# Kernel optimization log

Hardware: AMD Instinct MI355X
Metric: run time of the kernel (lower is better)

## Reference

```python
import jax, jax.numpy as jnp
import numpy as np

N, D_IN, D_H, N_HEADS, N_CLS = 8192, 384, 64, 4, 6
LN_EPS = 1e-5


def setup_inputs() -> dict:
    key = jax.random.key(0)
    ks = jax.random.split(key, 8)
    x = jax.random.normal(ks[0], (N, D_IN), dtype=jnp.float32)
    proj_w = jax.random.normal(ks[1], (D_IN, D_H), dtype=jnp.float32) / np.sqrt(D_IN)
    proj_b = jnp.zeros((D_H,), jnp.float32)
    head_w = jax.random.normal(ks[2], (N_HEADS, D_H, D_H), dtype=jnp.float32) / np.sqrt(D_H)
    head_b = jnp.zeros((N_HEADS, D_H), jnp.float32)
    attn_w = jnp.ones((N_HEADS,), jnp.float32)  # nn.Parameter(torch.ones(num_heads))
    gamma = jnp.ones((D_H,), jnp.float32)
    beta = jnp.zeros((D_H,), jnp.float32)
    fc_w = jax.random.normal(ks[3], (D_H, N_CLS), dtype=jnp.float32) / np.sqrt(D_H)
    fc_b = jnp.zeros((N_CLS,), jnp.float32)
    return {"x": x, "proj_w": proj_w, "proj_b": proj_b, "head_w": head_w,
            "head_b": head_b, "attn_w": attn_w, "gamma": gamma, "beta": beta,
            "fc_w": fc_w, "fc_b": fc_b}


def _safe_cdist_sq_to_dist(sq):
    # Euclidean distance with zero (sub)gradient at zero distance, matching torch.cdist.
    pos = sq > 0
    return jnp.where(pos, jnp.sqrt(jnp.where(pos, sq, 1.0)), 0.0)


def reference(x, proj_w, proj_b, head_w, head_b, attn_w, gamma, beta, fc_w, fc_b):
    h = jax.nn.relu(x @ proj_w + proj_b)                      # [N, D_H]
    hp = jnp.einsum('nd,hde->hne', h, head_w) + head_b[:, None, :]  # [H, N, D_H]
    sumsq = jnp.sum(hp * hp, axis=-1)                          # [H, N]
    sq = sumsq[:, :, None] + sumsq[:, None, :] - 2.0 * jnp.einsum('hnd,hmd->hnm', hp, hp)
    dist = _safe_cdist_sq_to_dist(jnp.maximum(sq, 0.0))        # [H, N, N]
    scores = jax.nn.softmax(-dist, axis=-1)                    # [H, N, N]
    h_head = jnp.einsum('hnm,hmd->hnd', scores, hp)            # [H, N, D_H]
    aw = jax.nn.softmax(attn_w, axis=0)                        # [H]
    combined = jnp.einsum('h,hnd->nd', aw, h_head)             # [N, D_H]
    mu = jnp.mean(combined, axis=-1, keepdims=True)
    var = jnp.mean((combined - mu) ** 2, axis=-1, keepdims=True)
    normed = (combined - mu) * jax.lax.rsqrt(var + LN_EPS) * gamma + beta
    return normed @ fc_w + fc_b                                # [N, N_CLS]
```

## Files before the change

### kernel.cpp

```cpp
#include <hip/hip_runtime.h>

#define N_TOK 8192
#define D_IN 384
#define D_H 64
#define NHEADS 4
#define NSPLIT 3
#define N_CLS 6
#define LN_EPS 1e-5f

typedef __attribute__((ext_vector_type(8))) short short8;
typedef __attribute__((ext_vector_type(4))) float f32x4;

#define L2E2 2.08136898100560774f

__device__ __forceinline__ unsigned short f2bf(float f) {
    unsigned int u = __float_as_uint(f);
    u += 0x7FFFu + ((u >> 16) & 1u);
    return (unsigned short)(u >> 16);
}
__device__ __forceinline__ float bf2f(unsigned short s) {
    return __uint_as_float(((unsigned int)s) << 16);
}

__device__ __forceinline__ int kperm(int k) {
    return (k & 32) + 2 * (k & 15) + ((k >> 4) & 1);
}

__global__ __launch_bounds__(512) void stage1_kernel(
    const float* __restrict__ x, const float* __restrict__ proj_w,
    const float* __restrict__ proj_b, const float* __restrict__ head_w,
    const float* __restrict__ head_b,
    unsigned short* __restrict__ hp, unsigned short* __restrict__ Vf,
    float* __restrict__ ssq2)
{
    const int lane = threadIdx.x & 63;
    const int wv   = threadIdx.x >> 6;
    const int rb0  = blockIdx.x * 32;

    __shared__ float h_sh[32][68];
    __shared__ __align__(16) unsigned short vt[NHEADS][4][64][8];

    {
        float acc[4];
        float b = proj_b[lane];
        #pragma unroll
        for (int r = 0; r < 4; ++r) acc[r] = b;
        const float* x0 = x + (size_t)(rb0 + wv * 4) * D_IN;
        #pragma unroll 2
        for (int k4 = 0; k4 < D_IN / 4; ++k4) {
            float w0 = proj_w[(k4 * 4 + 0) * 64 + lane];
            float w1 = proj_w[(k4 * 4 + 1) * 64 + lane];
            float w2 = proj_w[(k4 * 4 + 2) * 64 + lane];
            float w3 = proj_w[(k4 * 4 + 3) * 64 + lane];
            #pragma unroll
            for (int r = 0; r < 4; ++r) {
                float4 xv = *(const float4*)(x0 + r * D_IN + k4 * 4);
                acc[r] = fmaf(xv.x, w0, acc[r]);
                acc[r] = fmaf(xv.y, w1, acc[r]);
                acc[r] = fmaf(xv.z, w2, acc[r]);
                acc[r] = fmaf(xv.w, w3, acc[r]);
            }
        }
        #pragma unroll
        for (int r = 0; r < 4; ++r)
            h_sh[wv * 4 + r][lane] = fmaxf(acc[r], 0.f);
    }
    __syncthreads();

    const int head = wv >> 1;
    const int half = wv & 1;
    float a[16];
    {
        float b = head_b[head * 64 + lane];
        #pragma unroll
        for (int r = 0; r < 16; ++r) a[r] = b;
    }
    const float* wb = head_w + head * 64 * 64;
    #pragma unroll 2
    for (int e4 = 0; e4 < 16; ++e4) {
        float w0 = wb[(e4 * 4 + 0) * 64 + lane];
        float w1 = wb[(e4 * 4 + 1) * 64 + lane];
        float w2 = wb[(e4 * 4 + 2) * 64 + lane];
        float w3 = wb[(e4 * 4 + 3) * 64 + lane];
        #pragma unroll
        for (int r = 0; r < 16; ++r) {
            float4 hv = *(const float4*)&h_sh[half * 16 + r][e4 * 4];
            a[r] = fmaf(hv.x, w0, a[r]);
            a[r] = fmaf(hv.y, w1, a[r]);
            a[r] = fmaf(hv.z, w2, a[r]);
            a[r] = fmaf(hv.w, w3, a[r]);
        }
    }

    #pragma unroll
    for (int r = 0; r < 16; ++r) {
        int kl  = half * 16 + r;
        int row = rb0 + kl;
        unsigned short hb = f2bf(a[r]);
        float hf = bf2f(hb);
        hp[((size_t)head * N_TOK + row) * 64 + lane] = hb;
        int p = kperm(row & 63);
        vt[head][(p >> 3) & 3][lane][p & 7] = hb;
        float s = hf * hf;
        #pragma unroll
        for (int off = 32; off > 0; off >>= 1) s += __shfl_xor(s, off);
        if (lane == 0) ssq2[head * N_TOK + row] = s * L2E2;
    }
    __syncthreads();

    const int kgbase = (rb0 & 32) ? 4 : 0;
    #pragma unroll
    for (int i = 0; i < 2; ++i) {
        int c  = threadIdx.x + 512 * i;
        int hc = c >> 8, rem = c & 255;
        int kg = rem >> 6, d = rem & 63;
        short8 v = *(const short8*)&vt[hc][kg][d][0];
        *(short8*)&Vf[(((size_t)hc * (N_TOK / 8) + (rb0 >> 6) * 8 + kgbase + kg) * 64
                       + d) * 8] = v;
    }
}

__global__ __launch_bounds__(256, 4) void flash_kernel(
    const unsigned short* __restrict__ hp, const unsigned short* __restrict__ Vf,
    const float* __restrict__ ssq2, unsigned short* __restrict__ Og,
    float* __restrict__ Lg)
{
    const int head  = blockIdx.x & 3;
    const int split = blockIdx.x >> 2;
    const int q0    = blockIdx.y * 128;
    const int w     = threadIdx.x >> 6;
    const int lane  = threadIdx.x & 63;
    const int col   = lane & 15;
    const int quad  = lane >> 4;
    const int tid   = threadIdx.x;

    __shared__ __align__(16) unsigned short Psh[4][2][16][72];
    __shared__ __align__(16) unsigned short Kst[2][4096];
    __shared__ __align__(16) unsigned short Vst[2][4096];

    const unsigned short* hpH = hp + head * (N_TOK * 64);
    const unsigned short* VfH = Vf + head * (N_TOK * 64);
    const float* ssqH = ssq2 + head * N_TOK;

    const int rb = q0 + w * 32;
    const bool diag_lo = ((rb >> 5) & 1) == 0;

    short8 aQ[2][2];
    float ssqn2[2][4];
    #pragma unroll
    for (int s = 0; s < 2; ++s) {
        const unsigned short* qrow = hpH + (rb + s * 16 + col) * 64;
        aQ[s][0] = *(const short8*)(qrow + quad * 8);
        aQ[s][1] = *(const short8*)(qrow + 32 + quad * 8);
        #pragma unroll
        for (int r = 0; r < 4; ++r)
            ssqn2[s][r] = ssqH[rb + s * 16 + quad * 4 + r];
    }

    const f32x4 zero4 = {0.f, 0.f, 0.f, 0.f};
    f32x4 accO[2][4] = {{zero4, zero4, zero4, zero4}, {zero4, zero4, zero4, zero4}};
    f32x4 accL[2] = {zero4, zero4};
    const short8 ones = {16256,16256,16256,16256,16256,16256,16256,16256};
    const float NEG2L2 = -2.0f * L2E2;

    const int koff0 = (((tid & ~7) | ((tid & 7) ^ ((tid >> 3) & 7))) << 4);
    const int karow = col * 128 + ((quad ^ (col & 7)) << 4);
    const int va    = (quad * 64 + col) << 4;

    const int kt0   = (split * 128) / NSPLIT;
    const int ktend = ((split + 1) * 128) / NSPLIT;

    short8 stK0, stK1, stV0, stV1;
    {
        const unsigned short* kg = hpH + kt0 * 4096;
        const unsigned short* vg = VfH + kt0 * 4096;
        stK0 = *(const short8*)(kg + tid * 8);
        stK1 = *(const short8*)(kg + tid * 8 + 2048);
        stV0 = *(const short8*)(vg + tid * 8);
        stV1 = *(const short8*)(vg + tid * 8 + 2048);
        *(short8*)((char*)&Kst[0][0] + koff0)        = stK0;
        *(short8*)((char*)&Kst[0][0] + koff0 + 4096) = stK1;
        *(short8*)((char*)&Vst[0][0] + tid * 16)        = stV0;
        *(short8*)((char*)&Vst[0][0] + tid * 16 + 4096) = stV1;
    }
    float smc[4];
    #pragma unroll
    for (int nt = 0; nt < 4; ++nt) smc[nt] = ssqH[kt0 * 64 + nt * 16 + col];
    __syncthreads();

    #pragma unroll 1
    for (int kt = kt0; kt < ktend; ++kt) {
        const int b = (kt - kt0) & 1;
        const char* Kb = (const char*)&Kst[b][0];
        const char* Vb = (const char*)&Vst[b][0];
        const bool has_next = (kt + 1 < ktend);

        float smn[4];
        if (has_next) {
            const unsigned short* kg = hpH + (kt + 1) * 4096;
            const unsigned short* vg = VfH + (kt + 1) * 4096;
            stK0 = *(const short8*)(kg + tid * 8);
            stK1 = *(const short8*)(kg + tid * 8 + 2048);
            stV0 = *(const short8*)(vg + tid * 8);
            stV1 = *(const short8*)(vg + tid * 8 + 2048);
            #pragma unroll
            for (int nt = 0; nt < 4; ++nt)
                smn[nt] = ssqH[(kt + 1) * 64 + nt * 16 + col];
        }

        f32x4 aSA[2][2] = {{zero4, zero4}, {zero4, zero4}};
        {
            short8 k0 = *(const short8*)(Kb + karow);
            short8 k1 = *(const short8*)(Kb + (karow ^ 64));
            short8 k2 = *(const short8*)(Kb + 2048 + karow);
            short8 k3 = *(const short8*)(Kb + 2048 + (karow ^ 64));
            aSA[0][0] = __builtin_amdgcn_mfma_f32_16x16x32_bf16(aQ[0][0], k0, aSA[0][0], 0, 0, 0);
            aSA[0][0] = __builtin_amdgcn_mfma_f32_16x16x32_bf16(aQ[0][1], k1, aSA[0][0], 0, 0, 0);
            aSA[1][0] = __builtin_amdgcn_mfma_f32_16x16x32_bf16(aQ[1][0], k0, aSA[1][0], 0, 0, 0);
            aSA[1][0] = __builtin_amdgcn_mfma_f32_16x16x32_bf16(aQ[1][1], k1, aSA[1][0], 0, 0, 0);
            aSA[0][1] = __builtin_amdgcn_mfma_f32_16x16x32_bf16(aQ[0][0], k2, aSA[0][1], 0, 0, 0);
            aSA[0][1] = __builtin_amdgcn_mfma_f32_16x16x32_bf16(aQ[0][1], k3, aSA[0][1], 0, 0, 0);
            aSA[1][1] = __builtin_amdgcn_mfma_f32_16x16x32_bf16(aQ[1][0], k2, aSA[1][1], 0, 0, 0);
            aSA[1][1] = __builtin_amdgcn_mfma_f32_16x16x32_bf16(aQ[1][1], k3, aSA[1][1], 0, 0, 0);
        }

        #pragma unroll
        for (int s = 0; s < 2; ++s) {
            float pf0[4], pf1[4];
            #pragma unroll
            for (int r = 0; r < 4; ++r) {
                float sq0 = fmaf(aSA[s][0][r], NEG2L2, ssqn2[s][r] + smc[0]);
                pf0[r] = __builtin_amdgcn_exp2f(-__builtin_amdgcn_sqrtf(fmaxf(sq0, 0.f)));
                float sq1 = fmaf(aSA[s][1][r], NEG2L2, ssqn2[s][r] + smc[1]);
                pf1[r] = __builtin_amdgcn_exp2f(-__builtin_amdgcn_sqrtf(fmaxf(sq1, 0.f)));
            }
            #pragma unroll
            for (int r = 0; r < 4; ++r) {
                unsigned int d0 = __builtin_amdgcn_perm(__float_as_uint(pf1[r]),
                                                        __float_as_uint(pf0[r]), 0x07060302u);
                *(unsigned int*)&Psh[w][s][quad * 4 + r][2 * col] = d0;
            }
        }
        if (diag_lo && kt == (rb >> 6) && lane < 16) {
            #pragma unroll
            for (int s = 0; s < 2; ++s) {
                int t = ((rb + s * 16) >> 4) & 3;
                Psh[w][s][lane][2 * lane + (t & 1)] = 0x3F80;
            }
        }

        f32x4 aSB[2][2] = {{zero4, zero4}, {zero4, zero4}};
        {
            short8 k0 = *(const short8*)(Kb + 4096 + karow);
            short8 k1 = *(const short8*)(Kb + 4096 + (karow ^ 64));
            short8 k2 = *(const short8*)(Kb + 6144 + karow);
            short8 k3 = *(const short8*)(Kb + 6144 + (karow ^ 64));
            aSB[0][0] = __builtin_amdgcn_mfma_f32_16x16x32_bf16(aQ[0][0], k0, aSB[0][0], 0, 0, 0);
            aSB[0][0] = __builtin_amdgcn_mfma_f32_16x16x32_bf16(aQ[0][1], k1, aSB[0][0], 0, 0, 0);
            aSB[1][0] = __builtin_amdgcn_mfma_f32_16x16x32_bf16(aQ[1][0], k0, aSB[1][0], 0, 0, 0);
            aSB[1][0] = __builtin_amdgcn_mfma_f32_16x16x32_bf16(aQ[1][1], k1, aSB[1][0], 0, 0, 0);
            aSB[0][1] = __builtin_amdgcn_mfma_f32_16x16x32_bf16(aQ[0][0], k2, aSB[0][1], 0, 0, 0);
            aSB[0][1] = __builtin_amdgcn_mfma_f32_16x16x32_bf16(aQ[0][1], k3, aSB[0][1], 0, 0, 0);
            aSB[1][1] = __builtin_amdgcn_mfma_f32_16x16x32_bf16(aQ[1][0], k2, aSB[1][1], 0, 0, 0);
            aSB[1][1] = __builtin_amdgcn_mfma_f32_16x16x32_bf16(aQ[1][1], k3, aSB[1][1], 0, 0, 0);
        }

        #pragma unroll
        for (int s = 0; s < 2; ++s) {
            float pf2[4], pf3[4];
            #pragma unroll
            for (int r = 0; r < 4; ++r) {
                float sq2 = fmaf(aSB[s][0][r], NEG2L2, ssqn2[s][r] + smc[2]);
                pf2[r] = __builtin_amdgcn_exp2f(-__builtin_amdgcn_sqrtf(fmaxf(sq2, 0.f)));
                float sq3 = fmaf(aSB[s][1][r], NEG2L2, ssqn2[s][r] + smc[3]);
                pf3[r] = __builtin_amdgcn_exp2f(-__builtin_amdgcn_sqrtf(fmaxf(sq3, 0.f)));
            }
            #pragma unroll
            for (int r = 0; r < 4; ++r) {
                unsigned int d1 = __builtin_amdgcn_perm(__float_as_uint(pf3[r]),
                                                        __float_as_uint(pf2[r]), 0x07060302u);
                *(unsigned int*)&Psh[w][s][quad * 4 + r][32 + 2 * col] = d1;
            }
        }
        if (!diag_lo && kt == (rb >> 6) && lane < 16) {
            #pragma unroll
            for (int s = 0; s < 2; ++s) {
                int t = ((rb + s * 16) >> 4) & 3;
                Psh[w][s][lane][32 + 2 * lane + (t & 1)] = 0x3F80;
            }
        }

        {
            short8 aP0 = *(const short8*)&Psh[w][0][col][quad * 8];
            short8 aP1 = *(const short8*)&Psh[w][1][col][quad * 8];
            short8 bV[4];
            #pragma unroll
            for (int dt = 0; dt < 4; ++dt)
                bV[dt] = *(const short8*)(Vb + va + dt * 256);
            accL[0] = __builtin_amdgcn_mfma_f32_16x16x32_bf16(aP0, ones, accL[0], 0, 0, 0);
            accL[1] = __builtin_amdgcn_mfma_f32_16x16x32_bf16(aP1, ones, accL[1], 0, 0, 0);
            #pragma unroll
            for (int dt = 0; dt < 4; ++dt) {
                accO[0][dt] = __builtin_amdgcn_mfma_f32_16x16x32_bf16(aP0, bV[dt], accO[0][dt], 0, 0, 0);
                accO[1][dt] = __builtin_amdgcn_mfma_f32_16x16x32_bf16(aP1, bV[dt], accO[1][dt], 0, 0, 0);
            }
        }
        {
            short8 aP0b = *(const short8*)&Psh[w][0][col][32 + quad * 8];
            short8 aP1b = *(const short8*)&Psh[w][1][col][32 + quad * 8];
            short8 bV[4];
            #pragma unroll
            for (int dt = 0; dt < 4; ++dt)
                bV[dt] = *(const short8*)(Vb + va + dt * 256 + 4096);
            accL[0] = __builtin_amdgcn_mfma_f32_16x16x32_bf16(aP0b, ones, accL[0], 0, 0, 0);
            accL[1] = __builtin_amdgcn_mfma_f32_16x16x32_bf16(aP1b, ones, accL[1], 0, 0, 0);
            #pragma unroll
            for (int dt = 0; dt < 4; ++dt) {
                accO[0][dt] = __builtin_amdgcn_mfma_f32_16x16x32_bf16(aP0b, bV[dt], accO[0][dt], 0, 0, 0);
                accO[1][dt] = __builtin_amdgcn_mfma_f32_16x16x32_bf16(aP1b, bV[dt], accO[1][dt], 0, 0, 0);
            }
        }

        if (has_next) {
            char* Kn = (char*)&Kst[b ^ 1][0];
            char* Vn = (char*)&Vst[b ^ 1][0];
            *(short8*)(Kn + koff0)        = stK0;
            *(short8*)(Kn + koff0 + 4096) = stK1;
            *(short8*)(Vn + tid * 16)        = stV0;
            *(short8*)(Vn + tid * 16 + 4096) = stV1;
        }
        __syncthreads();
        if (has_next) {
            smc[0] = smn[0]; smc[1] = smn[1]; smc[2] = smn[2]; smc[3] = smn[3];
        }
    }

    unsigned short* og = Og + (size_t)(split * NHEADS + head) * N_TOK * 64;
    float* lg = Lg + (size_t)(split * NHEADS + head) * N_TOK;
    #pragma unroll
    for (int s = 0; s < 2; ++s)
        #pragma unroll
        for (int r = 0; r < 4; ++r) {
            int row = rb + s * 16 + quad * 4 + r;
            #pragma unroll
            for (int dt = 0; dt < 4; ++dt)
                og[row * 64 + dt * 16 + col] = f2bf(accO[s][dt][r]);
            if (col == 0) lg[row] = accL[s][r];
        }
}

__global__ __launch_bounds__(256) void combine_kernel(
    const unsigned short* __restrict__ Og, const float* __restrict__ Lg,
    const float* __restrict__ attn_w, const float* __restrict__ gamma,
    const float* __restrict__ beta, const float* __restrict__ fc_w,
    const float* __restrict__ fc_b, float* __restrict__ out)
{
    const int lane = threadIdx.x & 63;
    const int ty   = threadIdx.x >> 6;
    const int row  = blockIdx.x * 4 + ty;

    float a0 = attn_w[0], a1 = attn_w[1], a2 = attn_w[2], a3 = attn_w[3];
    float m = fmaxf(fmaxf(a0, a1), fmaxf(a2, a3));
    float e0 = __expf(a0 - m), e1 = __expf(a1 - m), e2 = __expf(a2 - m), e3 = __expf(a3 - m);
    float inv = 1.f / (e0 + e1 + e2 + e3);
    float aw[4] = {e0 * inv, e1 * inv, e2 * inv, e3 * inv};

    float c = 0.f;
    #pragma unroll
    for (int hh = 0; hh < NHEADS; ++hh) {
        float l = 0.f, o = 0.f;
        #pragma unroll
        for (int s = 0; s < NSPLIT; ++s) {
            l += Lg[(s * NHEADS + hh) * N_TOK + row];
            o += bf2f(Og[(size_t)((s * NHEADS + hh) * N_TOK + row) * 64 + lane]);
        }
        c += aw[hh] * o * __builtin_amdgcn_rcpf(l);
    }

    float s = c;
    #pragma unroll
    for (int off = 32; off > 0; off >>= 1) s += __shfl_xor(s, off);
    float mu = s * (1.f / 64.f);
    float d = c - mu;
    float v = d * d;
    #pragma unroll
    for (int off = 32; off > 0; off >>= 1) v += __shfl_xor(v, off);
    float normed = d * rsqrtf(v * (1.f / 64.f) + LN_EPS) * gamma[lane] + beta[lane];

    float lg[N_CLS];
    #pragma unroll
    for (int cc = 0; cc < N_CLS; ++cc) {
        float p = normed * fc_w[lane * N_CLS + cc];
        #pragma unroll
        for (int off = 32; off > 0; off >>= 1) p += __shfl_xor(p, off);
        lg[cc] = p;
    }
    if (lane == 0) {
        #pragma unroll
        for (int cc = 0; cc < N_CLS; ++cc)
            out[row * N_CLS + cc] = lg[cc] + fc_b[cc];
    }
}

extern "C" void kernel_launch(void* const* d_in, const int* in_sizes, int n_in,
                              void* d_out, int out_size, void* d_ws, size_t ws_size,
                              hipStream_t stream)
{
    const float* x      = (const float*)d_in[0];
    const float* proj_w = (const float*)d_in[1];
    const float* proj_b = (const float*)d_in[2];
    const float* head_w = (const float*)d_in[3];
    const float* head_b = (const float*)d_in[4];
    const float* attn_w = (const float*)d_in[5];
    const float* gamma  = (const float*)d_in[6];
    const float* beta   = (const float*)d_in[7];
    const float* fc_w   = (const float*)d_in[8];
    const float* fc_b   = (const float*)d_in[9];
    float* out = (float*)d_out;

    char* ws = (char*)d_ws;
    unsigned short* hp = (unsigned short*)(ws);
    unsigned short* Vf = (unsigned short*)(ws + (4u << 20));
    float* ssq2 = (float*)(ws + (8u << 20));
    unsigned short* Og = (unsigned short*)(ws + (8u << 20) + (128u << 10));
    float* Lg   = (float*)(ws + (20u << 20) + (128u << 10));

    stage1_kernel<<<N_TOK / 32, 512, 0, stream>>>(x, proj_w, proj_b, head_w, head_b,
                                                  hp, Vf, ssq2);
    dim3 g2(NHEADS * NSPLIT, N_TOK / 128);
    flash_kernel<<<g2, 256, 0, stream>>>(hp, Vf, ssq2, Og, Lg);
    combine_kernel<<<N_TOK / 4, 256, 0, stream>>>(Og, Lg, attn_w, gamma, beta,
                                                  fc_w, fc_b, out);
}
```

Before: 229.4 us.

## Stream K/V tiles via direct global-to-LDS loads with single buffers and swizzled P

```diff
diff --git a/kernel.cpp b/kernel.cpp
--- a/kernel.cpp
+++ b/kernel.cpp
@@ -4,7 +4,7 @@
 #define D_IN 384
 #define D_H 64
 #define NHEADS 4
-#define NSPLIT 3
+#define NSPLIT 4
 #define N_CLS 6
 #define LN_EPS 1e-5f
 
@@ -24,6 +24,12 @@
 
 __device__ __forceinline__ int kperm(int k) {
     return (k & 32) + 2 * (k & 15) + ((k >> 4) & 1);
+}
+
+__device__ __forceinline__ void gload_lds16(const void* g, void* l) {
+    __builtin_amdgcn_global_load_lds(
+        (const __attribute__((address_space(1))) unsigned int*)g,
+        (__attribute__((address_space(3))) unsigned int*)l, 16, 0, 0);
 }
 
 __global__ __launch_bounds__(512) void stage1_kernel(
@@ -134,9 +140,9 @@
     const int quad  = lane >> 4;
     const int tid   = threadIdx.x;
 
-    __shared__ __align__(16) unsigned short Psh[4][2][16][72];
-    __shared__ __align__(16) unsigned short Kst[2][4096];
-    __shared__ __align__(16) unsigned short Vst[2][4096];
+    __shared__ __align__(16) unsigned short Psh[4][2][16][64];
+    __shared__ __align__(16) unsigned short Kst[4096];
+    __shared__ __align__(16) unsigned short Vst[4096];
 
     const unsigned short* hpH = hp + head * (N_TOK * 64);
     const unsigned short* VfH = Vf + head * (N_TOK * 64);
@@ -166,22 +172,16 @@
     const int koff0 = (((tid & ~7) | ((tid & 7) ^ ((tid >> 3) & 7))) << 4);
     const int karow = col * 128 + ((quad ^ (col & 7)) << 4);
     const int va    = (quad * 64 + col) << 4;
-
-    const int kt0   = (split * 128) / NSPLIT;
-    const int ktend = ((split + 1) * 128) / NSPLIT;
-
-    short8 stK0, stK1, stV0, stV1;
+    const int wcb   = quad * 512 + ((((col >> 2) ^ ((quad & 1) << 2)) << 4))
+                      + ((col & 3) << 2);
+
+    const int kt0   = split * 32;
+    const int ktend = kt0 + 32;
+
     {
-        const unsigned short* kg = hpH + kt0 * 4096;
-        const unsigned short* vg = VfH + kt0 * 4096;
-        stK0 = *(const short8*)(kg + tid * 8);
-        stK1 = *(const short8*)(kg + tid * 8 + 2048);
-        stV0 = *(const short8*)(vg + tid * 8);
-        stV1 = *(const short8*)(vg + tid * 8 + 2048);
-        *(short8*)((char*)&Kst[0][0] + koff0)        = stK0;
-        *(short8*)((char*)&Kst[0][0] + koff0 + 4096) = stK1;
-        *(short8*)((char*)&Vst[0][0] + tid * 16)        = stV0;
-        *(short8*)((char*)&Vst[0][0] + tid * 16 + 4096) = stV1;
+        const char* kg = (const char*)(hpH + kt0 * 4096);
+        gload_lds16(kg + koff0,        (char*)Kst + tid * 16);
+        gload_lds16(kg + koff0 + 4096, (char*)Kst + tid * 16 + 4096);
     }
     float smc[4];
     #pragma unroll
@@ -190,23 +190,21 @@
 
     #pragma unroll 1
     for (int kt = kt0; kt < ktend; ++kt) {
-        const int b = (kt - kt0) & 1;
-        const char* Kb = (const char*)&Kst[b][0];
-        const char* Vb = (const char*)&Vst[b][0];
         const bool has_next = (kt + 1 < ktend);
 
+        {
+            const char* vg = (const char*)(VfH + kt * 4096);
+            gload_lds16(vg + tid * 16,        (char*)Vst + tid * 16);
+            gload_lds16(vg + tid * 16 + 4096, (char*)Vst + tid * 16 + 4096);
+        }
         float smn[4];
         if (has_next) {
-            const unsigned short* kg = hpH + (kt + 1) * 4096;
-            const unsigned short* vg = VfH + (kt + 1) * 4096;
-            stK0 = *(const short8*)(kg + tid * 8);
-            stK1 = *(const short8*)(kg + tid * 8 + 2048);
-            stV0 = *(const short8*)(vg + tid * 8);
-            stV1 = *(const short8*)(vg + tid * 8 + 2048);
             #pragma unroll
             for (int nt = 0; nt < 4; ++nt)
                 smn[nt] = ssqH[(kt + 1) * 64 + nt * 16 + col];
         }
+
+        const char* Kb = (const char*)Kst;
 
         f32x4 aSA[2][2] = {{zero4, zero4}, {zero4, zero4}};
         {
@@ -226,6 +224,7 @@
 
         #pragma unroll
         for (int s = 0; s < 2; ++s) {
+            char* pB = (char*)&Psh[w][s][0][0];
             float pf0[4], pf1[4];
             #pragma unroll
             for (int r = 0; r < 4; ++r) {
@@ -238,14 +237,16 @@
             for (int r = 0; r < 4; ++r) {
                 unsigned int d0 = __builtin_amdgcn_perm(__float_as_uint(pf1[r]),
                                                         __float_as_uint(pf0[r]), 0x07060302u);
-                *(unsigned int*)&Psh[w][s][quad * 4 + r][2 * col] = d0;
+                *(unsigned int*)(pB + ((wcb ^ (r << 4)) + r * 128)) = d0;
             }
         }
         if (diag_lo && kt == (rb >> 6) && lane < 16) {
             #pragma unroll
             for (int s = 0; s < 2; ++s) {
                 int t = ((rb + s * 16) >> 4) & 3;
-                Psh[w][s][lane][2 * lane + (t & 1)] = 0x3F80;
+                int sc2 = 4 * lane + 2 * (t & 1);
+                int ad = lane * 128 + (((lane >> 2) ^ (lane & 7)) << 4) + (sc2 & 15);
+                *(unsigned short*)((char*)&Psh[w][s][0][0] + ad) = 0x3F80;
             }
         }
 
@@ -267,6 +268,7 @@
 
         #pragma unroll
         for (int s = 0; s < 2; ++s) {
+            char* pB = (char*)&Psh[w][s][0][0];
             float pf2[4], pf3[4];
             #pragma unroll
             for (int r = 0; r < 4; ++r) {
@@ -279,20 +281,33 @@
             for (int r = 0; r < 4; ++r) {
                 unsigned int d1 = __builtin_amdgcn_perm(__float_as_uint(pf3[r]),
                                                         __float_as_uint(pf2[r]), 0x07060302u);
-                *(unsigned int*)&Psh[w][s][quad * 4 + r][32 + 2 * col] = d1;
+                *(unsigned int*)(pB + (((wcb ^ (r << 4)) + r * 128) ^ 64)) = d1;
             }
         }
         if (!diag_lo && kt == (rb >> 6) && lane < 16) {
             #pragma unroll
             for (int s = 0; s < 2; ++s) {
                 int t = ((rb + s * 16) >> 4) & 3;
-                Psh[w][s][lane][32 + 2 * lane + (t & 1)] = 0x3F80;
-            }
+                int sc2 = 4 * lane + 2 * (t & 1);
+                int ad = (lane * 128 + (((lane >> 2) ^ (lane & 7)) << 4) + (sc2 & 15)) ^ 64;
+                *(unsigned short*)((char*)&Psh[w][s][0][0] + ad) = 0x3F80;
+            }
+        }
+
+        __syncthreads();
+
+        if (has_next) {
+            const char* kgn = (const char*)(hpH + (kt + 1) * 4096);
+            gload_lds16(kgn + koff0,        (char*)Kst + tid * 16);
+            gload_lds16(kgn + koff0 + 4096, (char*)Kst + tid * 16 + 4096);
         }
 
         {
-            short8 aP0 = *(const short8*)&Psh[w][0][col][quad * 8];
-            short8 aP1 = *(const short8*)&Psh[w][1][col][quad * 8];
+            const char* p0 = (const char*)&Psh[w][0][0][0];
+            const char* p1 = (const char*)&Psh[w][1][0][0];
+            const char* Vb = (const char*)Vst;
+            short8 aP0 = *(const short8*)(p0 + karow);
+            short8 aP1 = *(const short8*)(p1 + karow);
             short8 bV[4];
             #pragma unroll
             for (int dt = 0; dt < 4; ++dt)
@@ -304,11 +319,8 @@
                 accO[0][dt] = __builtin_amdgcn_mfma_f32_16x16x32_bf16(aP0, bV[dt], accO[0][dt], 0, 0, 0);
                 accO[1][dt] = __builtin_amdgcn_mfma_f32_16x16x32_bf16(aP1, bV[dt], accO[1][dt], 0, 0, 0);
             }
-        }
-        {
-            short8 aP0b = *(const short8*)&Psh[w][0][col][32 + quad * 8];
-            short8 aP1b = *(const short8*)&Psh[w][1][col][32 + quad * 8];
-            short8 bV[4];
+            short8 aP0b = *(const short8*)(p0 + (karow ^ 64));
+            short8 aP1b = *(const short8*)(p1 + (karow ^ 64));
             #pragma unroll
             for (int dt = 0; dt < 4; ++dt)
                 bV[dt] = *(const short8*)(Vb + va + dt * 256 + 4096);
@@ -321,14 +333,6 @@
             }
         }
 
-        if (has_next) {
-            char* Kn = (char*)&Kst[b ^ 1][0];
-            char* Vn = (char*)&Vst[b ^ 1][0];
-            *(short8*)(Kn + koff0)        = stK0;
-            *(short8*)(Kn + koff0 + 4096) = stK1;
-            *(short8*)(Vn + tid * 16)        = stV0;
-            *(short8*)(Vn + tid * 16 + 4096) = stV1;
-        }
         __syncthreads();
         if (has_next) {
             smc[0] = smn[0]; smc[1] = smn[1]; smc[2] = smn[2]; smc[3] = smn[3];
@@ -423,7 +427,7 @@
     unsigned short* Vf = (unsigned short*)(ws + (4u << 20));
     float* ssq2 = (float*)(ws + (8u << 20));
     unsigned short* Og = (unsigned short*)(ws + (8u << 20) + (128u << 10));
-    float* Lg   = (float*)(ws + (20u << 20) + (128u << 10));
+    float* Lg   = (float*)(ws + (24u << 20) + (128u << 10));
 
     stage1_kernel<<<N_TOK / 32, 512, 0, stream>>>(x, proj_w, proj_b, head_w, head_b,
                                                   hp, Vf, ssq2);
```

New measurement: 219.8 us. 4.2% less time.
